# Kernel tuning notes

Hardware: AMD Instinct MI355X
Metric: run time of the kernel (lower is better)

The kernel has to match this reference:

```python
import jax, jax.numpy as jnp
import numpy as np

SOS_TOKEN = 0


def setup_inputs() -> dict:
    key = jax.random.key(0)
    ks = jax.random.split(key, 16)
    B, S, T, H, V = 64, 64, 32, 512, 32000
    s = 1.0 / np.sqrt(H)
    inp = {
        "encoder_outputs": jax.random.normal(ks[0], (B, S, H), jnp.float32),
        "encoder_hidden": jax.random.normal(ks[1], (1, B, H), jnp.float32),
        "target_tensor": jax.random.randint(ks[2], (B, T), 0, V),
        "emb": jax.random.normal(ks[3], (V, H), jnp.float32),
        "Wa": jax.random.uniform(ks[4], (H, H), jnp.float32, -s, s),
        "ba": jnp.zeros((H,), jnp.float32),
        "Ua": jax.random.uniform(ks[5], (H, H), jnp.float32, -s, s),
        "bu": jnp.zeros((H,), jnp.float32),
        "va": jax.random.uniform(ks[6], (H, 1), jnp.float32, -s, s),
        "bv": jnp.zeros((1,), jnp.float32),
        "w_ih": jax.random.uniform(ks[7], (3 * H, 2 * H), jnp.float32, -s, s),
        "b_ih": jax.random.uniform(ks[8], (3 * H,), jnp.float32, -s, s),
        "w_hh": jax.random.uniform(ks[9], (3 * H, H), jnp.float32, -s, s),
        "b_hh": jax.random.uniform(ks[10], (3 * H,), jnp.float32, -s, s),
        "Wo": jax.random.uniform(ks[11], (V, H), jnp.float32, -s, s),
        "bo": jax.random.uniform(ks[12], (V,), jnp.float32, -s, s),
    }
    return inp


def _gru_cell(x, h, w_ih, b_ih, w_hh, b_hh):
    # x: [B, 2H], h: [B, H] -- PyTorch nn.GRU gate math
    H = h.shape[-1]
    gi = x @ w_ih.T + b_ih            # [B, 3H]
    gh = h @ w_hh.T + b_hh            # [B, 3H]
    i_r, i_z, i_n = gi[:, :H], gi[:, H:2 * H], gi[:, 2 * H:]
    h_r, h_z, h_n = gh[:, :H], gh[:, H:2 * H], gh[:, 2 * H:]
    r = jax.nn.sigmoid(i_r + h_r)
    z = jax.nn.sigmoid(i_z + h_z)
    n = jnp.tanh(i_n + r * h_n)
    return (1.0 - z) * n + z * h


def reference(encoder_outputs, encoder_hidden, target_tensor,
              emb, Wa, ba, Ua, bu, va, bv,
              w_ih, b_ih, w_hh, b_hh, Wo, bo):
    B, S, H = encoder_outputs.shape
    T = target_tensor.shape[1]
    # Teacher forcing: step t input is SOS for t=0 else target[:, t-1]
    sos = jnp.full((B, 1), SOS_TOKEN, dtype=target_tensor.dtype)
    input_ids = jnp.concatenate([sos, target_tensor[:, :-1]], axis=1)  # [B, T]
    embedded = emb[input_ids]  # [B, T, H]  (dropout is identity in eval)

    # Precompute key projection once (invariant across steps)
    Ua_keys = encoder_outputs @ Ua.T + bu  # [B, S, H]

    def step(h, x_emb):
        # Bahdanau additive attention: query = hidden state
        scores = jnp.tanh(h[:, None, :] @ Wa.T + ba + Ua_keys) @ va + bv  # [B, S, 1]
        scores = scores[..., 0]                                           # [B, S]
        attn = jax.nn.softmax(scores, axis=-1)
        context = jnp.einsum('bs,bsh->bh', attn, encoder_outputs)
        x = jnp.concatenate([x_emb, context], axis=-1)                    # [B, 2H]
        h_new = _gru_cell(x, h, w_ih, b_ih, w_hh, b_hh)
        logits = h_new @ Wo.T + bo                                        # [B, V]
        return h_new, (logits, attn)

    h0 = encoder_hidden[0]  # [B, H]
    h_final, (logits_t, attn_t) = jax.lax.scan(step, h0, jnp.swapaxes(embedded, 0, 1))
    logits = jnp.swapaxes(logits_t, 0, 1)        # [B, T, V]
    attentions = jnp.swapaxes(attn_t, 0, 1)      # [B, T, S]
    log_probs = jax.nn.log_softmax(logits, axis=-1)
    decoder_hidden = h_final[None]               # [1, B, H]
    return (log_probs, decoder_hidden, attentions)
```

## Files before the change

### kernel.cpp

```cpp
#include <hip/hip_runtime.h>

typedef unsigned short u16;
typedef __bf16 bf16x8 __attribute__((ext_vector_type(8)));
typedef float f32x4 __attribute__((ext_vector_type(4)));

#define Bsz 64
#define Ssz 64
#define Tsz 32
#define Hsz 512
#define Vsz 32000
#define NCONV 160
#define NTOT 256

static __device__ inline u16 f2bf(float f) {
    union { float f; unsigned u; } v; v.f = f;
    unsigned u = v.u;
    unsigned r = (u + 0x7FFFu + ((u >> 16) & 1u)) >> 16;
    return (u16)r;
}
static __device__ inline float bf2f(u16 v) {
    union { unsigned u; float f; } x; x.u = ((unsigned)v) << 16; return x.f;
}
static __device__ inline float tanh_fast(float x) {
    float e = __expf(2.f * x);
    return 1.f - 2.f / (e + 1.f);
}
static __device__ inline void st_u32(unsigned* p, unsigned v) {
    __hip_atomic_store(p, v, __ATOMIC_RELAXED, __HIP_MEMORY_SCOPE_AGENT);
}
static __device__ inline unsigned ld_u32(const unsigned* p) {
    return __hip_atomic_load(p, __ATOMIC_RELAXED, __HIP_MEMORY_SCOPE_AGENT);
}

#define GLOAD_LDS16(g, l) \
    __builtin_amdgcn_global_load_lds((const __attribute__((address_space(1))) void*)(g), \
                                     (__attribute__((address_space(3))) void*)(l), 16, 0, 0)

__global__ void prep_kernel(const float* __restrict__ enc, const float* __restrict__ Ua,
                            const float* __restrict__ Wa, const float* __restrict__ wih,
                            const float* __restrict__ whh, const float* __restrict__ ehid,
                            const int* __restrict__ target, const float* __restrict__ emb,
                            u16* __restrict__ encbf, u16* __restrict__ Uabf,
                            u16* __restrict__ Wabf, u16* __restrict__ wihbf,
                            u16* __restrict__ whhbf, u16* __restrict__ h0bf,
                            u16* __restrict__ xbuf) {
    const int n0 = 2097152, n1 = 262144, n2 = 262144, n3 = 1572864, n4 = 786432, n5 = 32768;
    const int n6 = Tsz * Bsz * Hsz;
    const int total = n0 + n1 + n2 + n3 + n4 + n5 + n6;
    for (int i = blockIdx.x * blockDim.x + threadIdx.x; i < total; i += gridDim.x * blockDim.x) {
        int j = i;
        if (j < n0) { encbf[j] = f2bf(enc[j]); continue; } j -= n0;
        if (j < n1) { Uabf[j] = f2bf(Ua[j]); continue; } j -= n1;
        if (j < n2) { Wabf[j] = f2bf(Wa[j]); continue; } j -= n2;
        if (j < n3) { wihbf[j] = f2bf(wih[j]); continue; } j -= n3;
        if (j < n4) { whhbf[j] = f2bf(whh[j]); continue; } j -= n4;
        if (j < n5) { h0bf[j] = f2bf(ehid[j]); continue; } j -= n5;
        {
            int t = j / (Bsz * Hsz);
            int rem = j % (Bsz * Hsz);
            int b = rem / Hsz, k = rem % Hsz;
            int id = (t == 0) ? 0 : target[b * Tsz + (t - 1)];
            xbuf[((size_t)t * Bsz + b) * 1024 + k] = f2bf(emb[(size_t)id * Hsz + k]);
        }
    }
}

__global__ __launch_bounds__(256) void gemm_bt(const u16* __restrict__ A, const u16* __restrict__ Bw,
                                               const float* __restrict__ bias, float* __restrict__ out,
                                               int M, int N, int K) {
    __shared__ __align__(16) u16 As[128 * 32];
    __shared__ __align__(16) u16 Bs[128 * 32];
    int m0 = blockIdx.x * 128, n0 = blockIdx.y * 128;
    int tid = threadIdx.x, lane = tid & 63, wid = tid >> 6;
    int wm = wid & 1, wn = wid >> 1;
    f32x4 acc[4][4] = {};
    for (int k0 = 0; k0 < K; k0 += 32) {
        int e0 = wid * 64 + lane;
        int e1 = e0 + 256;
        GLOAD_LDS16(&A[(size_t)(m0 + (e0 >> 2)) * K + k0 + (e0 & 3) * 8], (char*)As + wid * 1024);
        GLOAD_LDS16(&A[(size_t)(m0 + (e1 >> 2)) * K + k0 + (e1 & 3) * 8], (char*)As + 4096 + wid * 1024);
        GLOAD_LDS16(&Bw[(size_t)(n0 + (e0 >> 2)) * K + k0 + (e0 & 3) * 8], (char*)Bs + wid * 1024);
        GLOAD_LDS16(&Bw[(size_t)(n0 + (e1 >> 2)) * K + k0 + (e1 & 3) * 8], (char*)Bs + 4096 + wid * 1024);
        __syncthreads();
        bf16x8 av[4], bvv[4];
        for (int mi = 0; mi < 4; ++mi)
            av[mi] = *(const bf16x8*)&As[(wm * 64 + mi * 16 + (lane & 15)) * 32 + (lane >> 4) * 8];
        for (int ni = 0; ni < 4; ++ni)
            bvv[ni] = *(const bf16x8*)&Bs[(wn * 64 + ni * 16 + (lane & 15)) * 32 + (lane >> 4) * 8];
        for (int mi = 0; mi < 4; ++mi)
            for (int ni = 0; ni < 4; ++ni)
                acc[mi][ni] = __builtin_amdgcn_mfma_f32_16x16x32_bf16(av[mi], bvv[ni], acc[mi][ni], 0, 0, 0);
        __syncthreads();
    }
    for (int mi = 0; mi < 4; ++mi)
        for (int ni = 0; ni < 4; ++ni) {
            int n = n0 + wn * 64 + ni * 16 + (lane & 15);
            float bb = bias[n];
            for (int r = 0; r < 4; ++r) {
                int m = m0 + wm * 64 + mi * 16 + (lane >> 4) * 4 + r;
                out[(size_t)m * N + n] = acc[mi][ni][r] + bb;
            }
        }
}

static __device__ inline void arrive(unsigned* bar, int slot, unsigned val, int tid) {
    asm volatile("s_waitcnt vmcnt(0)" ::: "memory");
    __syncthreads();
    if (tid == 0) st_u32(&bar[slot * 32], val);
}
static __device__ inline void pollflags1(unsigned* bar, int base, int n, unsigned target, int tid) {
    if (tid < n) {
        unsigned* p = &bar[(base + tid) * 32];
        while (ld_u32(p) < target) asm volatile("s_sleep 1");
    }
    __syncthreads();
}

__global__ __launch_bounds__(512, 1) void coop_kernel(
    const float* __restrict__ uak,
    u16* __restrict__ xbuf, u16* __restrict__ Abf,
    const u16* __restrict__ h0bf, const u16* __restrict__ wihbf, const u16* __restrict__ whhbf,
    const u16* __restrict__ Wabf, const float* __restrict__ enc,
    const float* __restrict__ va, const float* __restrict__ bv, const float* __restrict__ ba,
    const float* __restrict__ b_ih, const float* __restrict__ b_hh,
    const float* __restrict__ ehid,
    const float* __restrict__ Wo, u16* __restrict__ Wobf,
    float* __restrict__ out, u16* __restrict__ partials,
    unsigned* __restrict__ bar) {
    __shared__ __align__(16) char lds[149504];
    __shared__ float WhL[512];
    __shared__ float scL[64];
    __shared__ float vaL[512];

    const size_t HID_OFF = (size_t)Bsz * Tsz * Vsz;
    const size_t ATT_OFF = HID_OFF + (size_t)Bsz * Hsz;

    int tid = threadIdx.x, lane = tid & 63, wid = tid >> 6;
    int ln15 = lane & 15, hi = lane >> 4;
    int bx = blockIdx.x;

    unsigned* xbufU = (unsigned*)xbuf;
    unsigned* AbfU = (unsigned*)Abf;
    unsigned* partU = (unsigned*)partials;

    if (bx < 64) {
        int b = bx;
        u16* uakL = (u16*)lds;
        u16* encL = (u16*)(lds + 65536);
        for (int i = tid; i < Ssz * Hsz; i += 512) {
            uakL[i] = f2bf(uak[(size_t)b * Ssz * Hsz + i]);
            encL[i] = f2bf(enc[(size_t)b * Ssz * Hsz + i]);
        }
        vaL[tid] = va[tid];
        float bvv = bv[0];
        float ba_t = ba[tid];
        int halfsel = tid & 1;
        __syncthreads();

        for (int t = 0; t < Tsz; ++t) {
            pollflags1(bar, 64, 32, (unsigned)(t + 1), tid);
            {
                float acc = ba_t;
                const unsigned* pb = partU + (size_t)b * 256 + (tid >> 1);
#pragma unroll
                for (int g = 0; g < 32; ++g) {
                    unsigned pw = ld_u32(pb + (size_t)g * 16384);
                    acc += bf2f((u16)(halfsel ? (pw >> 16) : (pw & 0xffff)));
                }
                WhL[tid] = acc;
            }
            __syncthreads();
            for (int si = 0; si < 8; ++si) {
                int s = wid * 8 + si;
                float a = 0.f;
#pragma unroll
                for (int ji = 0; ji < 8; ++ji) {
                    int j = lane + ji * 64;
                    float x = WhL[j] + bf2f(uakL[s * 512 + j]);
                    a += tanh_fast(x) * vaL[j];
                }
                for (int off = 32; off; off >>= 1) a += __shfl_down(a, off);
                if (lane == 0) scL[s] = a + bvv;
            }
            __syncthreads();
            if (wid == 0) {
                float x = scL[lane];
                float mx = x;
                for (int off = 32; off; off >>= 1) mx = fmaxf(mx, __shfl_xor(mx, off));
                float e = __expf(x - mx);
                float sm = e;
                for (int off = 32; off; off >>= 1) sm += __shfl_xor(sm, off);
                float at = e / sm;
                scL[lane] = at;
                out[ATT_OFF + ((size_t)b * Tsz + t) * Ssz + lane] = at;
            }
            __syncthreads();
            float c = 0.f;
            for (int s = 0; s < Ssz; ++s)
                c += scL[s] * bf2f(encL[s * 512 + tid]);
            unsigned me = (unsigned)f2bf(c);
            unsigned other = __shfl_xor(me, 1);
            if ((tid & 1) == 0)
                st_u32(&xbufU[((size_t)t * Bsz + b) * 512 + 256 + (tid >> 1)], me | (other << 16));
            arrive(bar, bx, (unsigned)(t + 1), tid);
        }
    } else if (bx < 96) {
        int g = bx - 64, jbase = g * 16;
        u16* hsl = (u16*)(lds + 147456);
        for (int i = tid; i < 6144; i += 512) {
            int row = i >> 7, c16 = i & 127;
            int Rg = (row >> 4) * 512 + jbase + (row & 15);
            uint4 v = *(const uint4*)&wihbf[(size_t)Rg * 1024 + c16 * 8];
            *(uint4*)(lds + row * 2048 + ((c16 * 16) ^ ((row & 7) << 4))) = v;
        }
        for (int i = tid; i < 3072; i += 512) {
            int row = i >> 6, c16 = i & 63;
            int Rg = (row >> 4) * 512 + jbase + (row & 15);
            uint4 v = *(const uint4*)&whhbf[(size_t)Rg * 512 + c16 * 8];
            *(uint4*)(lds + 98304 + row * 1024 + ((c16 * 16) ^ ((row & 7) << 4))) = v;
        }
        const char* wih_l = lds;
        const char* whh_l = lds + 98304;
        int j = jbase + ln15;
        float bir = b_ih[j] + b_hh[j];
        float biz = b_ih[512 + j] + b_hh[512 + j];
        float bin = b_ih[1024 + j];
        float bhn = b_hh[1024 + j];
        float hp0 = 0.f, hp1 = 0.f, hp2 = 0.f, hp3 = 0.f;
        if (wid < 4) {
            int m = wid;
            hp0 = ehid[(size_t)(m * 16 + hi * 4 + 0) * Hsz + j];
            hp1 = ehid[(size_t)(m * 16 + hi * 4 + 1) * Hsz + j];
            hp2 = ehid[(size_t)(m * 16 + hi * 4 + 2) * Hsz + j];
            hp3 = ehid[(size_t)(m * 16 + hi * 4 + 3) * Hsz + j];
        }
        int swz = (ln15 & 7) << 4;
        bf16x8 zfr = {};
        bf16x8 wfrag[4];
#pragma unroll
        for (int i = 0; i < 4; ++i) {
            int jp = (wid * 4 + i) * 16 + ln15;
            wfrag[i] = (hi < 2) ? *(const bf16x8*)&Wabf[(size_t)jp * 512 + jbase + hi * 8] : zfr;
        }
        for (int i = tid; i < 1024; i += 512)
            hsl[i] = h0bf[(size_t)(i >> 4) * 512 + jbase + (i & 15)];
        __syncthreads();
#pragma unroll
        for (int mt = 0; mt < 4; ++mt) {
            bf16x8 af = (hi < 2) ? *(const bf16x8*)&hsl[(mt * 16 + ln15) * 16 + hi * 8] : zfr;
#pragma unroll
            for (int i = 0; i < 4; ++i) {
                f32x4 pacc = {};
                pacc = __builtin_amdgcn_mfma_f32_16x16x32_bf16(af, wfrag[i], pacc, 0, 0, 0);
                int n0 = (wid * 4 + i) * 16;
#pragma unroll
                for (int r = 0; r < 4; ++r) {
                    int b = mt * 16 + hi * 4 + r;
                    unsigned me = (unsigned)f2bf(pacc[r]);
                    unsigned other = __shfl_xor(me, 1);
                    if ((ln15 & 1) == 0)
                        st_u32(&partU[((size_t)g * 64 + b) * 256 + ((n0 + ln15) >> 1)], me | (other << 16));
                }
            }
        }
        arrive(bar, bx, 1u, tid);

        for (int t = 0; t < Tsz; ++t) {
            const u16* hbt = t ? (Abf + (size_t)(t - 1) * Bsz * Hsz) : h0bf;
            f32x4 ar = {}, az = {}, ain = {}, ahn = {};
            if (wid < 4) {
                int m = wid;
#pragma unroll 8
                for (int k0 = 0; k0 < 16; ++k0) {
                    bf16x8 a = *(const bf16x8*)&xbuf[((size_t)t * Bsz + m * 16 + ln15) * 1024 + k0 * 32 + hi * 8];
                    int byteIn = k0 * 64 + hi * 16;
                    bf16x8 b0 = *(const bf16x8*)(wih_l + (0 + ln15) * 2048 + (byteIn ^ swz));
                    bf16x8 b1 = *(const bf16x8*)(wih_l + (16 + ln15) * 2048 + (byteIn ^ swz));
                    bf16x8 b2 = *(const bf16x8*)(wih_l + (32 + ln15) * 2048 + (byteIn ^ swz));
                    ar = __builtin_amdgcn_mfma_f32_16x16x32_bf16(a, b0, ar, 0, 0, 0);
                    az = __builtin_amdgcn_mfma_f32_16x16x32_bf16(a, b1, az, 0, 0, 0);
                    ain = __builtin_amdgcn_mfma_f32_16x16x32_bf16(a, b2, ain, 0, 0, 0);
                }
            }
            pollflags1(bar, 64, 32, (unsigned)(t + 1), tid);
            if (wid < 4) {
                int m = wid;
#pragma unroll 8
                for (int k0 = 0; k0 < 16; ++k0) {
                    bf16x8 a = *(const bf16x8*)&hbt[(size_t)(m * 16 + ln15) * 512 + k0 * 32 + hi * 8];
                    int byteIn = k0 * 64 + hi * 16;
                    bf16x8 b0 = *(const bf16x8*)(whh_l + (0 + ln15) * 1024 + (byteIn ^ swz));
                    bf16x8 b1 = *(const bf16x8*)(whh_l + (16 + ln15) * 1024 + (byteIn ^ swz));
                    bf16x8 b2 = *(const bf16x8*)(whh_l + (32 + ln15) * 1024 + (byteIn ^ swz));
                    ar = __builtin_amdgcn_mfma_f32_16x16x32_bf16(a, b0, ar, 0, 0, 0);
                    az = __builtin_amdgcn_mfma_f32_16x16x32_bf16(a, b1, az, 0, 0, 0);
                    ahn = __builtin_amdgcn_mfma_f32_16x16x32_bf16(a, b2, ahn, 0, 0, 0);
                }
                unsigned* p = &bar[(wid * 16 + ln15) * 32];
                while (ld_u32(p) < (unsigned)(t + 1)) asm volatile("s_sleep 1");
#pragma unroll 8
                for (int k0 = 16; k0 < 32; ++k0) {
                    bf16x8 a = *(const bf16x8*)&xbuf[((size_t)t * Bsz + m * 16 + ln15) * 1024 + k0 * 32 + hi * 8];
                    int byteIn = k0 * 64 + hi * 16;
                    bf16x8 b0 = *(const bf16x8*)(wih_l + (0 + ln15) * 2048 + (byteIn ^ swz));
                    bf16x8 b1 = *(const bf16x8*)(wih_l + (16 + ln15) * 2048 + (byteIn ^ swz));
                    bf16x8 b2 = *(const bf16x8*)(wih_l + (32 + ln15) * 2048 + (byteIn ^ swz));
                    ar = __builtin_amdgcn_mfma_f32_16x16x32_bf16(a, b0, ar, 0, 0, 0);
                    az = __builtin_amdgcn_mfma_f32_16x16x32_bf16(a, b1, az, 0, 0, 0);
                    ain = __builtin_amdgcn_mfma_f32_16x16x32_bf16(a, b2, ain, 0, 0, 0);
                }
                float hpv[4] = {hp0, hp1, hp2, hp3};
#pragma unroll
                for (int r = 0; r < 4; ++r) {
                    int b = m * 16 + hi * 4 + r;
                    float rg = 1.f / (1.f + __expf(-(ar[r] + bir)));
                    float zg = 1.f / (1.f + __expf(-(az[r] + biz)));
                    float ng = tanh_fast(ain[r] + bin + rg * (ahn[r] + bhn));
                    float hv = (1.f - zg) * ng + zg * hpv[r];
                    hpv[r] = hv;
                    u16 hb = f2bf(hv);
                    unsigned me = (unsigned)hb;
                    unsigned other = __shfl_xor(me, 1);
                    if ((ln15 & 1) == 0)
                        st_u32(&AbfU[((size_t)t * Bsz + b) * 256 + (j >> 1)], me | (other << 16));
                    hsl[b * 16 + ln15] = hb;
                    if (t == Tsz - 1) out[HID_OFF + (size_t)b * 512 + j] = hv;
                }
                hp0 = hpv[0]; hp1 = hpv[1]; hp2 = hpv[2]; hp3 = hpv[3];
            }
            __syncthreads();
#pragma unroll
            for (int mt = 0; mt < 4; ++mt) {
                bf16x8 af = (hi < 2) ? *(const bf16x8*)&hsl[(mt * 16 + ln15) * 16 + hi * 8] : zfr;
#pragma unroll
                for (int i = 0; i < 4; ++i) {
                    f32x4 pacc = {};
                    pacc = __builtin_amdgcn_mfma_f32_16x16x32_bf16(af, wfrag[i], pacc, 0, 0, 0);
                    int n0 = (wid * 4 + i) * 16;
#pragma unroll
                    for (int r = 0; r < 4; ++r) {
                        int b = mt * 16 + hi * 4 + r;
                        unsigned me = (unsigned)f2bf(pacc[r]);
                        unsigned other = __shfl_xor(me, 1);
                        if ((ln15 & 1) == 0)
                            st_u32(&partU[((size_t)g * 64 + b) * 256 + ((n0 + ln15) >> 1)], me | (other << 16));
                    }
                }
            }
            arrive(bar, bx, (unsigned)(t + 2), tid);
        }
    } else {
        const float4* W4 = (const float4*)Wo;
        for (int i = (bx - 96) * 512 + tid; i < (Vsz * Hsz) / 4; i += NCONV * 512) {
            float4 v = W4[i];
            ushort4 o;
            o.x = f2bf(v.x); o.y = f2bf(v.y); o.z = f2bf(v.z); o.w = f2bf(v.w);
            *(ushort4*)&Wobf[(size_t)i * 4] = o;
        }
    }
}

__global__ __launch_bounds__(512) void gemm_logits(const u16* __restrict__ Abf, const u16* __restrict__ Wobf,
                                                   const float* __restrict__ bo, float* __restrict__ out,
                                                   float* __restrict__ sumexp) {
    __shared__ __align__(16) char lds[49152];
    char* As0 = lds;
    char* Bs0 = lds + 8192;
    char* As1 = lds + 24576;
    char* Bs1 = lds + 32768;
    int tid = threadIdx.x, lane = tid & 63, wid = tid >> 6;
    int ln15 = lane & 15, hi = lane >> 4;
    int wm = wid & 1, wn = wid >> 1;
    int job = blockIdx.x;
    int m0 = (job / 125) * 128, n0 = (job % 125) * 256;
    f32x4 acc[4][4] = {};
    {
        int e0 = wid * 64 + lane, r = e0 >> 2, c8 = (e0 & 3) * 8;
        GLOAD_LDS16(&Abf[(size_t)(m0 + r) * 512 + c8], As0 + wid * 1024);
        GLOAD_LDS16(&Wobf[(size_t)(n0 + r) * 512 + c8], Bs0 + wid * 1024);
        GLOAD_LDS16(&Wobf[(size_t)(n0 + 128 + r) * 512 + c8], Bs0 + 8192 + wid * 1024);
    }
#pragma unroll 2
    for (int ks = 0; ks < 16; ++ks) {
        const u16* As = (const u16*)((ks & 1) ? As1 : As0);
        const u16* Bs = (const u16*)((ks & 1) ? Bs1 : Bs0);
        if (ks < 15) {
            char* Asn = (ks & 1) ? As0 : As1;
            char* Bsn = (ks & 1) ? Bs0 : Bs1;
            int e0 = wid * 64 + lane, r = e0 >> 2, c8 = (e0 & 3) * 8;
            int k0 = (ks + 1) * 32;
            GLOAD_LDS16(&Abf[(size_t)(m0 + r) * 512 + k0 + c8], Asn + wid * 1024);
            GLOAD_LDS16(&Wobf[(size_t)(n0 + r) * 512 + k0 + c8], Bsn + wid * 1024);
            GLOAD_LDS16(&Wobf[(size_t)(n0 + 128 + r) * 512 + k0 + c8], Bsn + 8192 + wid * 1024);
            asm volatile("s_waitcnt vmcnt(3)" ::: "memory");
        } else {
            asm volatile("s_waitcnt vmcnt(0)" ::: "memory");
        }
        __builtin_amdgcn_s_barrier();
        bf16x8 av[4], bvv[4];
        for (int mi = 0; mi < 4; ++mi)
            av[mi] = *(const bf16x8*)&As[(wm * 64 + mi * 16 + ln15) * 32 + hi * 8];
        for (int ni = 0; ni < 4; ++ni)
            bvv[ni] = *(const bf16x8*)&Bs[(wn * 64 + ni * 16 + ln15) * 32 + hi * 8];
        for (int mi = 0; mi < 4; ++mi)
            for (int ni = 0; ni < 4; ++ni)
                acc[mi][ni] = __builtin_amdgcn_mfma_f32_16x16x32_bf16(av[mi], bvv[ni], acc[mi][ni], 0, 0, 0);
        asm volatile("s_waitcnt lgkmcnt(0)" ::: "memory");
        __builtin_amdgcn_s_barrier();
    }
    float* eps = (float*)lds;
    float bb[4];
#pragma unroll
    for (int ni = 0; ni < 4; ++ni) bb[ni] = bo[n0 + wn * 64 + ni * 16 + ln15];
    for (int mi = 0; mi < 4; ++mi) {
        __syncthreads();
#pragma unroll
        for (int ni = 0; ni < 4; ++ni)
#pragma unroll
            for (int r = 0; r < 4; ++r)
                eps[(wm * 16 + hi * 4 + r) * 256 + wn * 64 + ni * 16 + ln15] = acc[mi][ni][r] + bb[ni];
        __syncthreads();
#pragma unroll
        for (int k = 0; k < 4; ++k) {
            int idx = k * 512 + tid;
            int l = idx >> 6, c4 = idx & 63;
            int m = m0 + (l >> 4) * 64 + mi * 16 + (l & 15);
            int t = m >> 6, b = m & 63;
            float4 v = *(float4*)&eps[l * 256 + c4 * 4];
            *(float4*)&out[((size_t)(b * Tsz + t)) * Vsz + n0 + c4 * 4] = v;
            float e = __expf(v.x) + __expf(v.y) + __expf(v.z) + __expf(v.w);
            for (int off = 32; off; off >>= 1) e += __shfl_down(e, off);
            if (lane == 0) atomicAdd(&sumexp[(m & 63) * Tsz + (m >> 6)], e);
        }
    }
}

__global__ void sub_kernel(float* __restrict__ out, const float* __restrict__ sumexp) {
    const int total4 = (Bsz * Tsz * Vsz) / 4;
    float4* o4 = (float4*)out;
    for (int i = blockIdx.x * blockDim.x + threadIdx.x; i < total4; i += gridDim.x * blockDim.x) {
        float l = __logf(sumexp[i / (Vsz / 4)]);
        float4 v = o4[i];
        v.x -= l; v.y -= l; v.z -= l; v.w -= l;
        o4[i] = v;
    }
}

extern "C" void kernel_launch(void* const* d_in, const int* in_sizes, int n_in,
                              void* d_out, int out_size, void* d_ws, size_t ws_size,
                              hipStream_t stream) {
    const float* enc   = (const float*)d_in[0];
    const float* ehid  = (const float*)d_in[1];
    const int*   target= (const int*)d_in[2];
    const float* emb   = (const float*)d_in[3];
    const float* Wa    = (const float*)d_in[4];
    const float* ba    = (const float*)d_in[5];
    const float* Ua    = (const float*)d_in[6];
    const float* bu    = (const float*)d_in[7];
    const float* va    = (const float*)d_in[8];
    const float* bv    = (const float*)d_in[9];
    const float* w_ih  = (const float*)d_in[10];
    const float* b_ih  = (const float*)d_in[11];
    const float* w_hh  = (const float*)d_in[12];
    const float* b_hh  = (const float*)d_in[13];
    const float* Wo    = (const float*)d_in[14];
    const float* bo    = (const float*)d_in[15];
    float* out = (float*)d_out;

    char* w = (char*)d_ws;
    float* uak    = (float*)w; w += (size_t)4096 * 512 * 4;
    float* sumexp = (float*)w; w += 8192;
    unsigned* bar = (unsigned*)w; w += 128 * 128;
    u16* xbuf     = (u16*)w;   w += (size_t)Tsz * Bsz * 1024 * 2;
    u16* Abf      = (u16*)w;   w += (size_t)Tsz * Bsz * Hsz * 2;
    u16* h0bf     = (u16*)w;   w += (size_t)Bsz * Hsz * 2;
    u16* partials = (u16*)w;   w += (size_t)32 * Bsz * Hsz * 2;
    u16* Wabf     = (u16*)w;   w += (size_t)Hsz * Hsz * 2;
    u16* encbf    = (u16*)w;   w += (size_t)4096 * 512 * 2;
    u16* Uabf     = (u16*)w;   w += (size_t)Hsz * Hsz * 2;
    u16* wihbf    = (u16*)w;   w += (size_t)1536 * 1024 * 2;
    u16* whhbf    = (u16*)w;   w += (size_t)1536 * 512 * 2;
    u16* Wobf     = (u16*)w;   w += (size_t)Vsz * 512 * 2;

    prep_kernel<<<2048, 256, 0, stream>>>(enc, Ua, Wa, w_ih, w_hh, ehid, target, emb,
                                          encbf, Uabf, Wabf, wihbf, whhbf, h0bf, xbuf);

    gemm_bt<<<dim3(32, 4), 256, 0, stream>>>(encbf, Uabf, bu, uak, 4096, 512, 512);

    hipMemsetAsync(bar, 0, 128 * 128, stream);
    hipMemsetAsync(sumexp, 0, 2048 * 4, stream);

    coop_kernel<<<NTOT, 512, 0, stream>>>(uak, xbuf, Abf, h0bf, wihbf, whhbf,
                                          Wabf, enc, va, bv, ba, b_ih, b_hh,
                                          ehid, Wo, Wobf, out, partials, bar);

    gemm_logits<<<2000, 512, 0, stream>>>(Abf, Wobf, bo, out, sumexp);

    sub_kernel<<<2048, 256, 0, stream>>>(out, sumexp);
}
```

Before: 844.9 us.

## Store intermediate logits as bf16 scratch and prefetch context activations in GRU step

The logits GEMM now writes bf16 logits to a scratch buffer, and the log-softmax subtract kernel reads them back and writes the fp32 output. The fp32 logits therefore no longer make a write-then-read-then-write round trip, which cuts intermediate memory traffic. The cost is bf16 rounding of the logits before the log-sum-exp subtraction, which loses precision. The bf16 path only runs when the workspace is large enough. Separately, the GRU input-context loop now loads all 16 activation vectors up front before the MFMA loop, to hide load latency.

```diff
diff --git a/kernel.cpp b/kernel.cpp
--- a/kernel.cpp
+++ b/kernel.cpp
@@ -298,16 +298,19 @@
                 }
                 unsigned* p = &bar[(wid * 16 + ln15) * 32];
                 while (ld_u32(p) < (unsigned)(t + 1)) asm volatile("s_sleep 1");
-#pragma unroll 8
-                for (int k0 = 16; k0 < 32; ++k0) {
-                    bf16x8 a = *(const bf16x8*)&xbuf[((size_t)t * Bsz + m * 16 + ln15) * 1024 + k0 * 32 + hi * 8];
-                    int byteIn = k0 * 64 + hi * 16;
+                bf16x8 actx[16];
+#pragma unroll
+                for (int k0 = 0; k0 < 16; ++k0)
+                    actx[k0] = *(const bf16x8*)&xbuf[((size_t)t * Bsz + m * 16 + ln15) * 1024 + (16 + k0) * 32 + hi * 8];
+#pragma unroll
+                for (int k0 = 0; k0 < 16; ++k0) {
+                    int byteIn = (16 + k0) * 64 + hi * 16;
                     bf16x8 b0 = *(const bf16x8*)(wih_l + (0 + ln15) * 2048 + (byteIn ^ swz));
                     bf16x8 b1 = *(const bf16x8*)(wih_l + (16 + ln15) * 2048 + (byteIn ^ swz));
                     bf16x8 b2 = *(const bf16x8*)(wih_l + (32 + ln15) * 2048 + (byteIn ^ swz));
-                    ar = __builtin_amdgcn_mfma_f32_16x16x32_bf16(a, b0, ar, 0, 0, 0);
-                    az = __builtin_amdgcn_mfma_f32_16x16x32_bf16(a, b1, az, 0, 0, 0);
-                    ain = __builtin_amdgcn_mfma_f32_16x16x32_bf16(a, b2, ain, 0, 0, 0);
+                    ar = __builtin_amdgcn_mfma_f32_16x16x32_bf16(actx[k0], b0, ar, 0, 0, 0);
+                    az = __builtin_amdgcn_mfma_f32_16x16x32_bf16(actx[k0], b1, az, 0, 0, 0);
+                    ain = __builtin_amdgcn_mfma_f32_16x16x32_bf16(actx[k0], b2, ain, 0, 0, 0);
                 }
                 float hpv[4] = {hp0, hp1, hp2, hp3};
 #pragma unroll
@@ -360,9 +363,10 @@
     }
 }
 
+template <int BF16OUT>
 __global__ __launch_bounds__(512) void gemm_logits(const u16* __restrict__ Abf, const u16* __restrict__ Wobf,
                                                    const float* __restrict__ bo, float* __restrict__ out,
-                                                   float* __restrict__ sumexp) {
+                                                   u16* __restrict__ scr, float* __restrict__ sumexp) {
     __shared__ __align__(16) char lds[49152];
     char* As0 = lds;
     char* Bs0 = lds + 8192;
@@ -427,7 +431,13 @@
             int m = m0 + (l >> 4) * 64 + mi * 16 + (l & 15);
             int t = m >> 6, b = m & 63;
             float4 v = *(float4*)&eps[l * 256 + c4 * 4];
-            *(float4*)&out[((size_t)(b * Tsz + t)) * Vsz + n0 + c4 * 4] = v;
+            if (BF16OUT) {
+                ushort4 o;
+                o.x = f2bf(v.x); o.y = f2bf(v.y); o.z = f2bf(v.z); o.w = f2bf(v.w);
+                *(ushort4*)&scr[((size_t)(b * Tsz + t)) * Vsz + n0 + c4 * 4] = o;
+            } else {
+                *(float4*)&out[((size_t)(b * Tsz + t)) * Vsz + n0 + c4 * 4] = v;
+            }
             float e = __expf(v.x) + __expf(v.y) + __expf(v.z) + __expf(v.w);
             for (int off = 32; off; off >>= 1) e += __shfl_down(e, off);
             if (lane == 0) atomicAdd(&sumexp[(m & 63) * Tsz + (m >> 6)], e);
@@ -443,6 +453,22 @@
         float4 v = o4[i];
         v.x -= l; v.y -= l; v.z -= l; v.w -= l;
         o4[i] = v;
+    }
+}
+
+__global__ void sub_bf16_kernel(const u16* __restrict__ scr, const float* __restrict__ sumexp,
+                                float* __restrict__ out) {
+    const int total8 = (Bsz * Tsz * Vsz) / 8;
+    for (int i = blockIdx.x * blockDim.x + threadIdx.x; i < total8; i += gridDim.x * blockDim.x) {
+        float l = __logf(sumexp[i / (Vsz / 8)]);
+        uint4 v = *(const uint4*)&scr[(size_t)i * 8];
+        float4 a, b;
+        a.x = bf2f((u16)v.x) - l;        a.y = bf2f((u16)(v.x >> 16)) - l;
+        a.z = bf2f((u16)v.y) - l;        a.w = bf2f((u16)(v.y >> 16)) - l;
+        b.x = bf2f((u16)v.z) - l;        b.y = bf2f((u16)(v.z >> 16)) - l;
+        b.z = bf2f((u16)v.w) - l;        b.w = bf2f((u16)(v.w >> 16)) - l;
+        *(float4*)&out[(size_t)i * 8] = a;
+        *(float4*)&out[(size_t)i * 8 + 4] = b;
     }
 }
 
@@ -481,6 +507,8 @@
     u16* wihbf    = (u16*)w;   w += (size_t)1536 * 1024 * 2;
     u16* whhbf    = (u16*)w;   w += (size_t)1536 * 512 * 2;
     u16* Wobf     = (u16*)w;   w += (size_t)Vsz * 512 * 2;
+    u16* scrbf    = (u16*)w;   w += (size_t)Bsz * Tsz * Vsz * 2;
+    const int use_bf16 = (ws_size >= (size_t)(w - (char*)d_ws));
 
     prep_kernel<<<2048, 256, 0, stream>>>(enc, Ua, Wa, w_ih, w_hh, ehid, target, emb,
                                           encbf, Uabf, Wabf, wihbf, whhbf, h0bf, xbuf);
@@ -494,7 +522,11 @@
                                           Wabf, enc, va, bv, ba, b_ih, b_hh,
                                           ehid, Wo, Wobf, out, partials, bar);
 
-    gemm_logits<<<2000, 512, 0, stream>>>(Abf, Wobf, bo, out, sumexp);
-
-    sub_kernel<<<2048, 256, 0, stream>>>(out, sumexp);
-}
+    if (use_bf16) {
+        gemm_logits<1><<<2000, 512, 0, stream>>>(Abf, Wobf, bo, out, scrbf, sumexp);
+        sub_bf16_kernel<<<2048, 256, 0, stream>>>(scrbf, sumexp, out);
+    } else {
+        gemm_logits<0><<<2000, 512, 0, stream>>>(Abf, Wobf, bo, out, scrbf, sumexp);
+        sub_kernel<<<2048, 256, 0, stream>>>(out, sumexp);
+    }
+}
```

Result: slower. 896.3 us (+6.1%).
